# Optimization experiments

Hardware: AMD Instinct MI355X
Metric: run time of the kernel (lower is better)

## Reference

```python
import jax, jax.numpy as jnp
import numpy as np
from jax import lax

B, P, D = 4, 8192, 512          # 4 point clouds, 8192 pts each, 512-dim features
SCALES = (1.0, 0.5, 0.25)
BIG = 1e10


def fps_indices(pos_b, n_samples):
    """Farthest-point sampling on one cloud. pos_b: [P,3] -> idx [n_samples].
    Deterministic start at index 0 (original uses a random start)."""
    n_pts = pos_b.shape[0]

    def step(carry, _):
        dist, far = carry                       # dist:[P], far: scalar int
        centroid = pos_b[far]                   # [3]
        d = jnp.sum((pos_b - centroid) ** 2, axis=-1)  # [P]
        dist = jnp.minimum(dist, d)
        new_far = jnp.argmax(dist).astype(jnp.int32)
        return (dist, new_far), far

    init = (jnp.full((n_pts,), BIG, dtype=pos_b.dtype), jnp.int32(0))
    _, idx = lax.scan(step, init, None, length=n_samples)
    return idx                                  # [n_samples] int32


def setup_inputs() -> dict:
    key = jax.random.key(0)
    k1, k2 = jax.random.split(key)
    x = jax.random.normal(k1, (B * P, D), dtype=jnp.float32)
    pos = jax.random.normal(k2, (B * P, 3), dtype=jnp.float32)
    batch_idx = jnp.repeat(jnp.arange(B, dtype=jnp.int64), P)  # sorted, equal-sized batches
    return {"x": x, "pos": pos, "batch_idx": batch_idx}


def reference(x, pos, batch_idx):
    # batch_idx is sorted with equal counts -> per-batch view is a reshape
    xb = x.reshape(B, P, D)
    pb = pos.reshape(B, P, 3)

    feats = [xb]          # scale == 1.0 keeps all points
    poss = [pb]
    for s in SCALES[1:]:
        n = max(1, int(P * s))
        idx = jax.vmap(lambda p: fps_indices(p, n))(pb)          # [B, n]
        feats.append(jnp.take_along_axis(xb, idx[:, :, None], axis=1))  # [B, n, D]
        poss.append(jnp.take_along_axis(pb, idx[:, :, None], axis=1))   # [B, n, 3]

    # 'concat' fusion: per-batch concat over scales, then concat over batches
    fused_x = jnp.concatenate(feats, axis=1).reshape(-1, D)
    fused_p = jnp.concatenate(poss, axis=1).reshape(-1, 3)
    return fused_x, fused_p
```

## Files before the change

### kernel.cpp

```cpp
#include <hip/hip_runtime.h>


constexpr int kB   = 4;
constexpr int kP   = 8192;
constexpr int kD   = 512;
constexpr int kN1  = 4096;
constexpr int kN2  = 2048;
constexpr int kS   = kP + kN1 + kN2;
constexpr int kT   = 512;
constexpr int kW   = kT / 64;
constexpr int kPts = kP / kT;
constexpr int kG   = 2;
constexpr int kGp  = kPts / kG;

typedef unsigned long long u64;
typedef unsigned u32;

template <int CTRL>
__device__ __forceinline__ u32 dpp1(u32 v) {
  return (u32)__builtin_amdgcn_update_dpp((int)v, (int)v, CTRL, 0xF, 0xF, false);
}

__device__ __forceinline__ void keymax(float& d, u32& l, u32& x, u32& y, u32& z,
                                       float od, u32 ol, u32 ox, u32 oy, u32 oz) {
  bool t = (od > d) || (od == d && ol > l);
  d = t ? od : d; l = t ? ol : l;
  x = t ? ox : x; y = t ? oy : y; z = t ? oz : z;
}

#define DPP_STAGE(CTRL)                                                     \
  {                                                                         \
    u32 pd = dpp1<CTRL>(__float_as_uint(kd));                               \
    u32 pl = dpp1<CTRL>(kl);                                                \
    u32 qx = dpp1<CTRL>(kx);                                                \
    u32 qy = dpp1<CTRL>(ky);                                                \
    u32 qz = dpp1<CTRL>(kz);                                                \
    keymax(kd, kl, kx, ky, kz, __uint_as_float(pd), pl, qx, qy, qz);        \
  }

#define DPP_REDUCE6()                                                       \
  DPP_STAGE(0xB1);                                      \
  DPP_STAGE(0x4E);                                      \
  DPP_STAGE(0x141);                                    \
  DPP_STAGE(0x140);                                         \
  DPP_STAGE(0x142);                                        \
  DPP_STAGE(0x143);

__global__ __launch_bounds__(kT, 2)
void fps_kernel(const float* __restrict__ pos, int* __restrict__ idx_out) {
  const int b    = blockIdx.x;
  const int tid  = threadIdx.x;
  const int wave = tid >> 6;
  const int lane = tid & 63;
  const float* pb = pos + (size_t)b * kP * 3;
  int* idx = idx_out + b * kN1;

  __shared__ __attribute__((aligned(16))) float lds_pos[kP * 3];
  __shared__ u32 lds_key[kP];
  __shared__ float lds_bb[kW][6];
  __shared__ __attribute__((aligned(16))) u32 wslot[2][kW][8];
  __shared__ float lds_c0[3];

  {
    const float4* src = reinterpret_cast<const float4*>(pb);
    float4* dst = reinterpret_cast<float4*>(lds_pos);
#pragma unroll
    for (int i = 0; i < (kP * 3 / 4) / kT; ++i)
      dst[tid + i * kT] = src[tid + i * kT];
  }
  __syncthreads();

  float mn0 = 1e30f, mn1 = 1e30f, mn2 = 1e30f;
  float mx0 = -1e30f, mx1 = -1e30f, mx2 = -1e30f;
  for (int i = tid; i < kP; i += kT) {
    float x = lds_pos[3 * i], y = lds_pos[3 * i + 1], z = lds_pos[3 * i + 2];
    mn0 = fminf(mn0, x); mx0 = fmaxf(mx0, x);
    mn1 = fminf(mn1, y); mx1 = fmaxf(mx1, y);
    mn2 = fminf(mn2, z); mx2 = fmaxf(mx2, z);
  }
#pragma unroll
  for (int m = 32; m >= 1; m >>= 1) {
    mn0 = fminf(mn0, __shfl_xor(mn0, m, 64)); mx0 = fmaxf(mx0, __shfl_xor(mx0, m, 64));
    mn1 = fminf(mn1, __shfl_xor(mn1, m, 64)); mx1 = fmaxf(mx1, __shfl_xor(mx1, m, 64));
    mn2 = fminf(mn2, __shfl_xor(mn2, m, 64)); mx2 = fmaxf(mx2, __shfl_xor(mx2, m, 64));
  }
  if (lane == 0) {
    lds_bb[wave][0] = mn0; lds_bb[wave][1] = mn1; lds_bb[wave][2] = mn2;
    lds_bb[wave][3] = mx0; lds_bb[wave][4] = mx1; lds_bb[wave][5] = mx2;
  }
  __syncthreads();
#pragma unroll
  for (int w = 0; w < kW; ++w) {
    mn0 = fminf(mn0, lds_bb[w][0]); mn1 = fminf(mn1, lds_bb[w][1]); mn2 = fminf(mn2, lds_bb[w][2]);
    mx0 = fmaxf(mx0, lds_bb[w][3]); mx1 = fmaxf(mx1, lds_bb[w][4]); mx2 = fmaxf(mx2, lds_bb[w][5]);
  }

  {
    const float i0 = 63.0f / fmaxf(mx0 - mn0, 1e-20f);
    const float i1 = 63.0f / fmaxf(mx1 - mn1, 1e-20f);
    const float i2 = 63.0f / fmaxf(mx2 - mn2, 1e-20f);
    for (int i = tid; i < kP; i += kT) {
      int qx = (int)((lds_pos[3 * i]     - mn0) * i0);
      int qy = (int)((lds_pos[3 * i + 1] - mn1) * i1);
      int qz = (int)((lds_pos[3 * i + 2] - mn2) * i2);
      qx = min(max(qx, 0), 63); qy = min(max(qy, 0), 63); qz = min(max(qz, 0), 63);
      u32 code = 0;
#pragma unroll
      for (int t = 0; t < 6; ++t)
        code |= (((u32)(qx >> t) & 1u) << (3 * t)) |
                (((u32)(qy >> t) & 1u) << (3 * t + 1)) |
                (((u32)(qz >> t) & 1u) << (3 * t + 2));
      lds_key[i] = (code << 13) | (u32)i;
    }
  }
  __syncthreads();

  for (int kk = 2; kk <= kP; kk <<= 1) {
    for (int j = kk >> 1; j > 0; j >>= 1) {
      const int mask = j - 1;
#pragma unroll
      for (int it = 0; it < (kP / 2) / kT; ++it) {
        int i = tid + it * kT;
        int a = ((i & ~mask) << 1) | (i & mask);
        int c = a | j;
        u32 x = lds_key[a], y = lds_key[c];
        bool up = ((a & kk) == 0);
        if ((x > y) == up) { lds_key[a] = y; lds_key[c] = x; }
      }
      __syncthreads();
    }
  }

  float px[kPts], py[kPts], pz[kPts], dist_[kPts];
  u32 lo1_[kPts];
  {
    const int base = tid * kPts;
#pragma unroll
    for (int m = 0; m < kPts; ++m) {
      int o = (int)(lds_key[base + m] & 8191u);
      px[m] = lds_pos[3 * o];
      py[m] = lds_pos[3 * o + 1];
      pz[m] = lds_pos[3 * o + 2];
      lo1_[m] = (u32)(8192 - o);
      dist_[m] = 1e10f;
      if (o == 0) { lds_c0[0] = px[m]; lds_c0[1] = py[m]; lds_c0[2] = pz[m]; }
    }
  }

  float blx[kG], bhx[kG], bly[kG], bhy[kG], blz[kG], bhz[kG];
  float cgd[kG]; u32 cgl[kG], cgx[kG], cgy[kG], cgz[kG];
#pragma unroll
  for (int g = 0; g < kG; ++g) {
    float lx = 1e30f, hx = -1e30f, ly = 1e30f, hy = -1e30f, lz = 1e30f, hz = -1e30f;
    u32 lob = 0, wx = 0, wy = 0, wz = 0;
#pragma unroll
    for (int k = 0; k < kGp; ++k) {
      const int m = g * kGp + k;
      lx = fminf(lx, px[m]); hx = fmaxf(hx, px[m]);
      ly = fminf(ly, py[m]); hy = fmaxf(hy, py[m]);
      lz = fminf(lz, pz[m]); hz = fmaxf(hz, pz[m]);
      bool t = lo1_[m] > lob;
      lob = t ? lo1_[m] : lob;
      wx = t ? __float_as_uint(px[m]) : wx;
      wy = t ? __float_as_uint(py[m]) : wy;
      wz = t ? __float_as_uint(pz[m]) : wz;
    }
    blx[g] = lx; bhx[g] = hx; bly[g] = ly; bhy[g] = hy; blz[g] = lz; bhz[g] = hz;
    cgd[g] = 1e10f; cgl[g] = lob; cgx[g] = wx; cgy[g] = wy; cgz[g] = wz;
  }

  float wlx = fminf(blx[0], blx[1]), whx = fmaxf(bhx[0], bhx[1]);
  float wly = fminf(bly[0], bly[1]), why = fmaxf(bhy[0], bhy[1]);
  float wlz = fminf(blz[0], blz[1]), whz = fmaxf(bhz[0], bhz[1]);
#pragma unroll
  for (int m = 32; m >= 1; m >>= 1) {
    wlx = fminf(wlx, __shfl_xor(wlx, m, 64)); whx = fmaxf(whx, __shfl_xor(whx, m, 64));
    wly = fminf(wly, __shfl_xor(wly, m, 64)); why = fmaxf(why, __shfl_xor(why, m, 64));
    wlz = fminf(wlz, __shfl_xor(wlz, m, 64)); whz = fmaxf(whz, __shfl_xor(whz, m, 64));
  }

  float wkd; u32 wkl, wkx, wky, wkz;
  {
    float kd = cgd[0]; u32 kl = cgl[0], kx = cgx[0], ky = cgy[0], kz = cgz[0];
    keymax(kd, kl, kx, ky, kz, cgd[1], cgl[1], cgx[1], cgy[1], cgz[1]);
    DPP_REDUCE6();
    wkd = kd; wkl = kl; wkx = kx; wky = ky; wkz = kz;
  }
  __syncthreads();

  float cx = lds_c0[0], cy = lds_c0[1], cz = lds_c0[2];
  float wall = 1e10f;
  int far = 0;
  for (int s = 0; ; ++s) {
    if (tid == 0) idx[s] = far;
    if (s == kN1 - 1) break;

    float gxw = fmaxf(fmaxf(wlx - cx, cx - whx), 0.0f);
    float gyw = fmaxf(fmaxf(wly - cy, cy - why), 0.0f);
    float gzw = fmaxf(fmaxf(wlz - cz, cz - whz), 0.0f);
    float lb2w = gxw * gxw + gyw * gyw; lb2w = lb2w + gzw * gzw;

    if (!(lb2w * 0.999995f >= wall)) {
#pragma unroll
      for (int g = 0; g < kG; ++g) {
        float gx = fmaxf(fmaxf(blx[g] - cx, cx - bhx[g]), 0.0f);
        float gy = fmaxf(fmaxf(bly[g] - cy, cy - bhy[g]), 0.0f);
        float gz = fmaxf(fmaxf(blz[g] - cz, cz - bhz[g]), 0.0f);
        float lb2 = gx * gx + gy * gy; lb2 = lb2 + gz * gz;
        if (!(lb2 * 0.999995f >= cgd[g])) {
          {
#pragma clang fp contract(off)
#pragma unroll
            for (int k = 0; k < kGp; ++k) {
              const int m = g * kGp + k;
              float dx = px[m] - cx;
              float dy = py[m] - cy;
              float dz = pz[m] - cz;
              float d = dx * dx + dy * dy;
              d = d + dz * dz;
              dist_[m] = fminf(dist_[m], d);
            }
          }
          float vb = dist_[g * kGp];
#pragma unroll
          for (int k = 1; k < kGp; ++k) vb = fmaxf(vb, dist_[g * kGp + k]);
          u32 lob = 0;
#pragma unroll
          for (int k = 0; k < kGp; ++k) {
            const int m = g * kGp + k;
            u32 c = (dist_[m] == vb) ? lo1_[m] : 0u;
            lob = lob > c ? lob : c;
          }
          u32 wx = cgx[g], wy = cgy[g], wz = cgz[g];
#pragma unroll
          for (int k = 0; k < kGp; ++k) {
            const int m = g * kGp + k;
            bool t = (lo1_[m] == lob);
            wx = t ? __float_as_uint(px[m]) : wx;
            wy = t ? __float_as_uint(py[m]) : wy;
            wz = t ? __float_as_uint(pz[m]) : wz;
          }
          cgd[g] = vb; cgl[g] = lob; cgx[g] = wx; cgy[g] = wy; cgz[g] = wz;
        }
      }

      float kd = cgd[0]; u32 kl = cgl[0], kx = cgx[0], ky = cgy[0], kz = cgz[0];
      keymax(kd, kl, kx, ky, kz, cgd[1], cgl[1], cgx[1], cgy[1], cgz[1]);
      DPP_REDUCE6();
      wkd = kd; wkl = kl; wkx = kx; wky = ky; wkz = kz;
    }

    if (lane == 63) {
      u32* slot = &wslot[s & 1][wave][0];
      slot[0] = __float_as_uint(wkd); slot[1] = wkl;
      slot[2] = wkx; slot[3] = wky; slot[4] = wkz;
    }
    __syncthreads();

    const u32 (*sl)[8] = wslot[s & 1];
    float sd[kW]; u32 sv[kW], sx[kW], sy[kW], sz[kW];
#pragma unroll
    for (int w = 0; w < kW; ++w) {
      uint4 q = *reinterpret_cast<const uint4*>(&sl[w][0]);
      sd[w] = __uint_as_float(q.x); sv[w] = q.y;
      sx[w] = q.z; sy[w] = q.w; sz[w] = sl[w][4];
    }
    wall = __uint_as_float(sl[wave][0]);
#pragma unroll
    for (int st = 1; st < kW; st <<= 1)
#pragma unroll
      for (int w = 0; w < kW; w += 2 * st)
        keymax(sd[w], sv[w], sx[w], sy[w], sz[w],
               sd[w + st], sv[w + st], sx[w + st], sy[w + st], sz[w + st]);

    far = 8192 - (int)sv[0];
    cx = __uint_as_float(sx[0]);
    cy = __uint_as_float(sy[0]);
    cz = __uint_as_float(sz[0]);
  }
}

constexpr int kXRows     = kB * kS;
constexpr int kXBlocks   = kXRows / 2;
constexpr int kPosElems  = kB * kS * 3;
constexpr int kPosBlocks = kPosElems / 256;

__device__ __forceinline__ int src_row(int b, int r, const int* __restrict__ idx) {
  int s;
  if (r < kP)            s = r;
  else if (r < kP + kN1) s = idx[b * kN1 + (r - kP)];
  else                   s = idx[b * kN1 + (r - kP - kN1)];
  return b * kP + s;
}

__global__ __launch_bounds__(256)
void gather_kernel(const float* __restrict__ x, const float* __restrict__ pos,
                   const int* __restrict__ idx, float* __restrict__ out) {
  const int blk = blockIdx.x;
  if (blk < kXBlocks) {
    const int row  = blk * 2 + (threadIdx.x >> 7);
    const int lane = threadIdx.x & 127;
    const int b = row / kS;
    const int r = row - b * kS;
    const int sr = src_row(b, r, idx);
    const float4* src4 = reinterpret_cast<const float4*>(x + (size_t)sr * kD);
    float4* dst4       = reinterpret_cast<float4*>(out + (size_t)row * kD);
    dst4[lane] = src4[lane];
  } else {
    const int e = (blk - kXBlocks) * 256 + threadIdx.x;
    const int row = e / 3;
    const int c   = e - row * 3;
    const int b = row / kS;
    const int r = row - b * kS;
    const int sr = src_row(b, r, idx);
    float* outp = out + (size_t)kB * kS * kD;
    outp[e] = pos[sr * 3 + c];
  }
}

extern "C" void kernel_launch(void* const* d_in, const int* in_sizes, int n_in,
                              void* d_out, int out_size, void* d_ws, size_t ws_size,
                              hipStream_t stream) {
  const float* x   = (const float*)d_in[0];
  const float* pos = (const float*)d_in[1];
  int* idx = (int*)d_ws;

  fps_kernel<<<kB, kT, 0, stream>>>(pos, idx);
  gather_kernel<<<kXBlocks + kPosBlocks, 256, 0, stream>>>(x, pos, idx, (float*)d_out);
}
```

Before: 7.605 ms.

## Reduce cross-wave slots with DPP in low lanes and buffer FPS indices in LDS

After the barrier, each wave now loads only its lane's slot (lanes 0-7) and reduces the 8 wave candidates with three DPP stages, then broadcasts the winner with readfirstlane. Before, every lane loaded all 8 slots and ran a full keymax tree. The per-wave bound 'wall' now comes from a readlane of the wave's own reduced key instead of an LDS read. Selected indices are written to lds_key during the loop and copied to global memory with vectorized stores at the end. This shortens the serial per-iteration critical path, but it relies on the DPP row-shift pattern covering exactly 8 lanes correctly and on reusing lds_key for the indices.

```diff
diff --git a/kernel.cpp b/kernel.cpp
--- a/kernel.cpp
+++ b/kernel.cpp
@@ -46,6 +46,16 @@
   DPP_STAGE(0x142);                                        \
   DPP_STAGE(0x143);
 
+#define DPP_SLOT_STAGE(CTRL)                                                \
+  {                                                                         \
+    u32 pd = dpp1<CTRL>(__float_as_uint(sd));                               \
+    u32 pl = dpp1<CTRL>(sv);                                                \
+    u32 qx = dpp1<CTRL>(sx);                                                \
+    u32 qy = dpp1<CTRL>(sy);                                                \
+    u32 qz = dpp1<CTRL>(sz);                                                \
+    keymax(sd, sv, sx, sy, sz, __uint_as_float(pd), pl, qx, qy, qz);        \
+  }
+
 __global__ __launch_bounds__(kT, 2)
 void fps_kernel(const float* __restrict__ pos, int* __restrict__ idx_out) {
   const int b    = blockIdx.x;
@@ -56,7 +66,7 @@
   int* idx = idx_out + b * kN1;
 
   __shared__ __attribute__((aligned(16))) float lds_pos[kP * 3];
-  __shared__ u32 lds_key[kP];
+  __shared__ __attribute__((aligned(16))) u32 lds_key[kP];
   __shared__ float lds_bb[kW][6];
   __shared__ __attribute__((aligned(16))) u32 wslot[2][kW][8];
   __shared__ float lds_c0[3];
@@ -192,7 +202,7 @@
   float wall = 1e10f;
   int far = 0;
   for (int s = 0; ; ++s) {
-    if (tid == 0) idx[s] = far;
+    if (tid == 0) lds_key[s] = (u32)far;
     if (s == kN1 - 1) break;
 
     float gxw = fmaxf(fmaxf(wlx - cx, cx - whx), 0.0f);
@@ -248,6 +258,7 @@
       keymax(kd, kl, kx, ky, kz, cgd[1], cgl[1], cgx[1], cgy[1], cgz[1]);
       DPP_REDUCE6();
       wkd = kd; wkl = kl; wkx = kx; wky = ky; wkz = kz;
+      wall = __uint_as_float(__builtin_amdgcn_readlane(__float_as_uint(wkd), 63));
     }
 
     if (lane == 63) {
@@ -257,26 +268,29 @@
     }
     __syncthreads();
 
-    const u32 (*sl)[8] = wslot[s & 1];
-    float sd[kW]; u32 sv[kW], sx[kW], sy[kW], sz[kW];
-#pragma unroll
-    for (int w = 0; w < kW; ++w) {
-      uint4 q = *reinterpret_cast<const uint4*>(&sl[w][0]);
-      sd[w] = __uint_as_float(q.x); sv[w] = q.y;
-      sx[w] = q.z; sy[w] = q.w; sz[w] = sl[w][4];
-    }
-    wall = __uint_as_float(sl[wave][0]);
-#pragma unroll
-    for (int st = 1; st < kW; st <<= 1)
-#pragma unroll
-      for (int w = 0; w < kW; w += 2 * st)
-        keymax(sd[w], sv[w], sx[w], sy[w], sz[w],
-               sd[w + st], sv[w + st], sx[w + st], sy[w + st], sz[w + st]);
-
-    far = 8192 - (int)sv[0];
-    cx = __uint_as_float(sx[0]);
-    cy = __uint_as_float(sy[0]);
-    cz = __uint_as_float(sz[0]);
+    float sd = 0.0f; u32 sv = 0, sx = 0, sy = 0, sz = 0;
+    if (lane < kW) {
+      const u32* slot = &wslot[s & 1][lane][0];
+      uint4 q = *reinterpret_cast<const uint4*>(slot);
+      sd = __uint_as_float(q.x); sv = q.y;
+      sx = q.z; sy = q.w; sz = slot[4];
+      DPP_SLOT_STAGE(0xB1);
+      DPP_SLOT_STAGE(0x4E);
+      DPP_SLOT_STAGE(0x141);
+    }
+    far = 8192 - (int)__builtin_amdgcn_readfirstlane((int)sv);
+    cx = __uint_as_float(__builtin_amdgcn_readfirstlane((int)sx));
+    cy = __uint_as_float(__builtin_amdgcn_readfirstlane((int)sy));
+    cz = __uint_as_float(__builtin_amdgcn_readfirstlane((int)sz));
+  }
+
+  __syncthreads();
+  {
+    const uint4* src = reinterpret_cast<const uint4*>(lds_key);
+    uint4* dst = reinterpret_cast<uint4*>(idx);
+#pragma unroll
+    for (int i = 0; i < (kN1 / 4) / kT; ++i)
+      dst[tid + i * kT] = src[tid + i * kT];
   }
 }
 
```

Result: no change. 7.460 ms (-1.9%).
